# Kernel tuning notes

Measured on AMD Instinct MI355X. Metric: run time of the kernel, lower is better.

The kernel has to match this reference:

```python
import jax, jax.numpy as jnp
import numpy as np

# PEPS geometry (matches init_kwargs descriptor)
LX, LY, D, PHYS = 6, 6, 4, 2
BATCH = 1024


def _amplitude(T, xs):
    """Exact amplitude of one spin configuration.

    T : [Lx, Ly, d, D, D, D, D] site tensors, bond axes ordered (up, right, down, left).
    xs: [Lx, Ly] int spin configuration.
    Boundary (dangling) bonds of the open-boundary PEPS are index 0 of the
    corresponding axis (sliced away), exactly reproducing quimb's isel +
    contract_boundary_from_ymin/ymax (chi chosen >= exact rank) + contract.
    """
    ii = jnp.arange(LX)[:, None]
    jj = jnp.arange(LY)[None, :]
    A = T[ii, jj, xs]  # gather physical index -> [Lx, Ly, D, D, D, D]

    def site(i, j):
        a = A[i, j]  # [u, r, dn, l]
        if i == 0:
            a = a[0:1]            # top row: up bond is trivial
        if i == LX - 1:
            a = a[:, :, 0:1]      # bottom row: down bond is trivial
        return a

    # --- boundary MPS from ymin: absorb columns 0 .. Ly/2-1 ---
    # env tensor per row: [a, h, b] with a/b vertical MPS bonds, h the
    # horizontal bond facing the next (rightward) column.
    L = [site(i, 0)[:, :, :, 0] for i in range(LX)]  # l bond trivial -> [u, r, dn]
    for j in range(1, LY // 2):
        newL = []
        for i in range(LX):
            e = jnp.einsum('alb,urdl->aurbd', L[i], site(i, j))
            a, u, r, b, d = e.shape
            newL.append(e.reshape(a * u, r, b * d))
        L = newL

    # --- boundary MPS from ymax: absorb columns Ly-1 .. Ly/2 ---
    R = [jnp.transpose(site(i, LY - 1)[:, 0], (0, 2, 1)) for i in range(LX)]  # [u, l, dn]
    for j in range(LY - 2, LY // 2 - 1, -1):
        newR = []
        for i in range(LX):
            e = jnp.einsum('ahb,uhdl->aulbd', R[i], site(i, j))
            a, u, l, b, d = e.shape
            newR.append(e.reshape(a * u, l, b * d))
        R = newR

    # --- zip the two boundary MPS together row by row ---
    v = jnp.ones((1, 1), dtype=T.dtype)
    for i in range(LX):
        v = jnp.einsum('xy,xhz,yhw->zw', v, L[i], R[i])
    return v[0, 0]


def setup_inputs() -> dict:
    key = jax.random.key(0)
    k1, k2 = jax.random.split(key)
    # 0.35 scale keeps the product of 36 tensors numerically tame in fp32
    T = jax.random.normal(k1, (LX, LY, PHYS, D, D, D, D), dtype=jnp.float32) * 0.35
    x = jax.random.randint(k2, (BATCH, LX * LY), 0, PHYS, dtype=jnp.int32)
    return {"x": x, "T": T}


def reference(x, T):
    xs = x.reshape(-1, LX, LY)
    return jax.vmap(lambda s: _amplitude(T, s))(xs)  # [B] amplitudes
```

## Files before the change

### kernel.cpp

```cpp
#include <hip/hip_runtime.h>

#define NROW 6
#define NCOL 6
#define BATCH 1024
#define NSITE 36

__device__ __forceinline__ int SWZ(int a) { return a ^ (((a >> 5) & 7) << 2); }

typedef const float __attribute__((address_space(4))) * fcp;

__global__ void peps_reorder_kernel(const float* __restrict__ T,
                                    float* __restrict__ Tm)
{
    int idx = blockIdx.x * 256 + threadIdx.x;
    if (idx >= NSITE * 2 * 256) return;
    int i  = idx & 15;
    int o  = (idx >> 4) & 15;
    int sp = (idx >> 8) & 1;
    int st = idx >> 9;
    int g = i >> 2, x = i & 3, gp = o >> 2, z = o & 3;
    Tm[idx] = T[st * 512 + sp * 256 + x * 64 + gp * 16 + z * 4 + g];
}

template<int GIN, int GOUT, int XS, int ZS, bool C0>
__device__ __forceinline__ void do_step4(float* __restrict__ W, const fcp Msf,
                                         const int* __restrict__ A, int p4c,
                                         bool act)
{
    if (!act) return;
    float in_s[4][16];
    if (C0) {
        if (XS == 4) {
            #pragma unroll
            for (int i = 0; i < 4; ++i) {
                float4 q = *(const float4*)&W[A[i]];
                in_s[i][0] = q.x; in_s[i][1] = q.y;
                in_s[i][2] = q.z; in_s[i][3] = q.w;
            }
        } else {
            #pragma unroll
            for (int i = 0; i < 4; ++i) in_s[i][0] = W[A[i]];
        }
    } else if (ZS == 4) {
        #pragma unroll
        for (int g = 0; g < GIN; ++g)
            #pragma unroll
            for (int x = 0; x < XS; ++x) {
                float4 q = *(const float4*)&W[A[x] + g * 4096];
                in_s[0][g*4+x] = q.x; in_s[1][g*4+x] = q.y;
                in_s[2][g*4+x] = q.z; in_s[3][g*4+x] = q.w;
            }
    } else {
        #pragma unroll
        for (int g = 0; g < GIN; ++g)
            #pragma unroll
            for (int x = 0; x < XS; ++x)
                #pragma unroll
                for (int i = 0; i < 4; ++i)
                    in_s[i][g*4+x] = W[SWZ(x * p4c + A[i]) + g * 4096];
    }
    #pragma unroll
    for (int gp = 0; gp < GOUT; ++gp) {
        float a[ZS][4];
        #pragma unroll
        for (int z = 0; z < ZS; ++z) {
            const int mb = (gp * 4 + z) * 16;
            #pragma unroll
            for (int i = 0; i < 4; ++i) a[z][i] = 0.f;
            #pragma unroll
            for (int g = 0; g < GIN; ++g)
                #pragma unroll
                for (int x = 0; x < XS; ++x) {
                    const float m = Msf[mb + g * 4 + x];
                    #pragma unroll
                    for (int i = 0; i < 4; ++i)
                        a[z][i] += m * in_s[i][g*4+x];
                }
        }
        if (C0 && ZS == 4) {
            #pragma unroll
            for (int i = 0; i < 4; ++i)
                *(float4*)&W[A[i] + gp * 4096] =
                    make_float4(a[0][i], a[1][i], a[2][i], a[3][i]);
        } else if (ZS == 4) {
            #pragma unroll
            for (int z = 0; z < 4; ++z)
                *(float4*)&W[A[z] + gp * 4096] =
                    make_float4(a[z][0], a[z][1], a[z][2], a[z][3]);
        } else if (C0) {
            #pragma unroll
            for (int i = 0; i < 4; ++i) W[A[i] + gp * 4096] = a[0][i];
        } else {
            #pragma unroll
            for (int i = 0; i < 4; ++i) W[SWZ(A[i]) + gp * 4096] = a[0][i];
        }
    }
}

__global__ __launch_bounds__(256, 2)
void peps_amp_kernel(const int* __restrict__ X, const float* __restrict__ Tm,
                     float* __restrict__ out)
{
    __shared__ float W[16384];

    const int b = blockIdx.x;
    const int t = threadIdx.x;
    const int u0 = 4 * t;
    const int* xrow = X + b * NSITE;

    unsigned long long sm = 0ull;
    const int4* xp = (const int4*)xrow;
    #pragma unroll
    for (int k = 0; k < 9; ++k) {
        int4 v = xp[k];
        sm |= ((unsigned long long)(v.x & 1)) << (4 * k + 0);
        sm |= ((unsigned long long)(v.y & 1)) << (4 * k + 1);
        sm |= ((unsigned long long)(v.z & 1)) << (4 * k + 2);
        sm |= ((unsigned long long)(v.w & 1)) << (4 * k + 3);
    }
    {
        unsigned lo = __builtin_amdgcn_readfirstlane((int)(sm & 0xffffffffull));
        unsigned hi = __builtin_amdgcn_readfirstlane((int)(sm >> 32));
        sm = ((unsigned long long)hi << 32) | lo;
    }

    if (t == 0) W[0] = 1.0f;

    int step = 0;
    for (int row = 0; row < NROW; ++row) {
        const int xs = (row == 0) ? 1 : 4;
        const int zs = (row == NROW - 1) ? 1 : 4;
        for (int c = 0; c < NCOL; ++c, ++step) {
            const int lowb  = (zs == 4) ? 2 * c : 0;
            const int highb = (xs == 4) ? 2 * (5 - c) : 0;
            const int scount = 1 << (lowb + highb);
            const int p4c = 1 << (2 * c);
            const int lowmask = (1 << lowb) - 1;
            const bool act = (u0 < scount);

            const int spin = (int)((sm >> step) & 1ull);
            const fcp Msf = (fcp)(unsigned long long)
                (const void*)(Tm + (size_t)(step * 2 + spin) * 256);

            __syncthreads();

            int A[4];
            if (c == 0) {
                #pragma unroll
                for (int i = 0; i < 4; ++i) A[i] = SWZ(16 * t + 4 * i);
            } else if (zs == 4) {
                const int mr0 = ((u0 >> lowb) << (2 * c + 2)) | (u0 & lowmask);
                #pragma unroll
                for (int d = 0; d < 4; ++d) A[d] = SWZ(d * p4c + mr0);
            } else {
                #pragma unroll
                for (int i = 0; i < 4; ++i) A[i] = (u0 + i) << (2 * c + 2);
            }

            if (row == 0) {
                if (c == 0)            do_step4<1,4,1,4,true >(W, Msf, A, p4c, act);
                else if (c < NCOL - 1) do_step4<4,4,1,4,false>(W, Msf, A, p4c, act);
                else                   do_step4<4,1,1,4,false>(W, Msf, A, p4c, act);
            } else if (row < NROW - 1) {
                if (c == 0)            do_step4<1,4,4,4,true >(W, Msf, A, p4c, act);
                else if (c < NCOL - 1) do_step4<4,4,4,4,false>(W, Msf, A, p4c, act);
                else                   do_step4<4,1,4,4,false>(W, Msf, A, p4c, act);
            } else {
                if (c == 0)            do_step4<1,4,4,1,true >(W, Msf, A, p4c, act);
                else if (c < NCOL - 1) do_step4<4,4,4,1,false>(W, Msf, A, p4c, act);
                else                   do_step4<4,1,4,1,false>(W, Msf, A, p4c, act);
            }
        }
    }
    __syncthreads();
    if (t == 0) out[b] = W[0];
}

extern "C" void kernel_launch(void* const* d_in, const int* in_sizes, int n_in,
                              void* d_out, int out_size, void* d_ws, size_t ws_size,
                              hipStream_t stream) {
    const int*   X  = (const int*)d_in[0];
    const float* Tg = (const float*)d_in[1];
    float* out = (float*)d_out;
    float* Tm  = (float*)d_ws;
    (void)in_sizes; (void)n_in; (void)ws_size; (void)out_size;
    peps_reorder_kernel<<<dim3(72), dim3(256), 0, stream>>>(Tg, Tm);
    peps_amp_kernel<<<dim3(BATCH), dim3(256), 0, stream>>>(X, Tm, out);
}
```

Measured before the change: 200.7 us.

## Fuse pairs of site contractions per thread to halve barrier count

Replaces the generic per-site step loop with specialized routines that contract two adjacent sites per thread while the intermediate stays in registers. This halves the number of shared-memory round trips and __syncthreads barriers per row. The first and last rows get dedicated small-thread-count code paths. The swizzle function gains an extra XOR term to reduce LDS bank conflicts for the new access strides. The cost is higher register pressure from the 64-element intermediates and more specialized code to maintain.

```diff
diff --git a/kernel.cpp b/kernel.cpp
--- a/kernel.cpp
+++ b/kernel.cpp
@@ -5,9 +5,18 @@
 #define BATCH 1024
 #define NSITE 36
 
-__device__ __forceinline__ int SWZ(int a) { return a ^ (((a >> 5) & 7) << 2); }
+__device__ __forceinline__ int SWZ(int a) {
+    return a ^ (((a >> 5) & 7) << 2) ^ (((a >> 8) & 3) << 3);
+}
 
 typedef const float __attribute__((address_space(4))) * fcp;
+
+__device__ __forceinline__ fcp msel(const float* Tm, int step,
+                                    unsigned long long sm) {
+    int spin = (int)((sm >> step) & 1ull);
+    return (fcp)(unsigned long long)(const void*)
+        (Tm + (size_t)(step * 2 + spin) * 256);
+}
 
 __global__ void peps_reorder_kernel(const float* __restrict__ T,
                                     float* __restrict__ Tm)
@@ -22,79 +31,92 @@
     Tm[idx] = T[st * 512 + sp * 256 + x * 64 + gp * 16 + z * 4 + g];
 }
 
-template<int GIN, int GOUT, int XS, int ZS, bool C0>
-__device__ __forceinline__ void do_step4(float* __restrict__ W, const fcp Msf,
-                                         const int* __restrict__ A, int p4c,
-                                         bool act)
+__device__ __forceinline__ void mid_first(float* __restrict__ W, fcp M0,
+                                          fcp M1, int base)
 {
-    if (!act) return;
-    float in_s[4][16];
-    if (C0) {
-        if (XS == 4) {
-            #pragma unroll
-            for (int i = 0; i < 4; ++i) {
-                float4 q = *(const float4*)&W[A[i]];
-                in_s[i][0] = q.x; in_s[i][1] = q.y;
-                in_s[i][2] = q.z; in_s[i][3] = q.w;
-            }
-        } else {
-            #pragma unroll
-            for (int i = 0; i < 4; ++i) in_s[i][0] = W[A[i]];
-        }
-    } else if (ZS == 4) {
-        #pragma unroll
-        for (int g = 0; g < GIN; ++g)
-            #pragma unroll
-            for (int x = 0; x < XS; ++x) {
-                float4 q = *(const float4*)&W[A[x] + g * 4096];
-                in_s[0][g*4+x] = q.x; in_s[1][g*4+x] = q.y;
-                in_s[2][g*4+x] = q.z; in_s[3][g*4+x] = q.w;
-            }
-    } else {
-        #pragma unroll
-        for (int g = 0; g < GIN; ++g)
-            #pragma unroll
-            for (int x = 0; x < XS; ++x)
-                #pragma unroll
-                for (int i = 0; i < 4; ++i)
-                    in_s[i][g*4+x] = W[SWZ(x * p4c + A[i]) + g * 4096];
-    }
-    #pragma unroll
-    for (int gp = 0; gp < GOUT; ++gp) {
-        float a[ZS][4];
-        #pragma unroll
-        for (int z = 0; z < ZS; ++z) {
-            const int mb = (gp * 4 + z) * 16;
-            #pragma unroll
-            for (int i = 0; i < 4; ++i) a[z][i] = 0.f;
-            #pragma unroll
-            for (int g = 0; g < GIN; ++g)
-                #pragma unroll
-                for (int x = 0; x < XS; ++x) {
-                    const float m = Msf[mb + g * 4 + x];
-                    #pragma unroll
-                    for (int i = 0; i < 4; ++i)
-                        a[z][i] += m * in_s[i][g*4+x];
-                }
-        }
-        if (C0 && ZS == 4) {
-            #pragma unroll
-            for (int i = 0; i < 4; ++i)
-                *(float4*)&W[A[i] + gp * 4096] =
-                    make_float4(a[0][i], a[1][i], a[2][i], a[3][i]);
-        } else if (ZS == 4) {
-            #pragma unroll
-            for (int z = 0; z < 4; ++z)
-                *(float4*)&W[A[z] + gp * 4096] =
-                    make_float4(a[z][0], a[z][1], a[z][2], a[z][3]);
-        } else if (C0) {
-            #pragma unroll
-            for (int i = 0; i < 4; ++i) W[A[i] + gp * 4096] = a[0][i];
-        } else {
-            #pragma unroll
-            for (int i = 0; i < 4; ++i) W[SWZ(A[i]) + gp * 4096] = a[0][i];
-        }
-    }
+    float U[4][4];
+    #pragma unroll
+    for (int x1 = 0; x1 < 4; ++x1) {
+        float4 q = *(const float4*)&W[SWZ(base + 4 * x1)];
+        U[x1][0] = q.x; U[x1][1] = q.y; U[x1][2] = q.z; U[x1][3] = q.w;
+    }
+    float V[4][4][4];
+    #pragma unroll
+    for (int gp = 0; gp < 4; ++gp)
+        #pragma unroll
+        for (int z0 = 0; z0 < 4; ++z0)
+            #pragma unroll
+            for (int x1 = 0; x1 < 4; ++x1) {
+                float acc = 0.f;
+                #pragma unroll
+                for (int x0 = 0; x0 < 4; ++x0)
+                    acc += M0[(gp * 4 + z0) * 16 + x0] * U[x1][x0];
+                V[gp][z0][x1] = acc;
+            }
+    #pragma unroll
+    for (int gp1 = 0; gp1 < 4; ++gp1)
+        #pragma unroll
+        for (int z1 = 0; z1 < 4; ++z1) {
+            float o[4];
+            #pragma unroll
+            for (int z0 = 0; z0 < 4; ++z0) {
+                float acc = 0.f;
+                #pragma unroll
+                for (int gp = 0; gp < 4; ++gp)
+                    #pragma unroll
+                    for (int x1 = 0; x1 < 4; ++x1)
+                        acc += M1[(gp1 * 4 + z1) * 16 + gp * 4 + x1]
+                             * V[gp][z0][x1];
+                o[z0] = acc;
+            }
+            *(float4*)&W[gp1 * 4096 + SWZ(base + 4 * z1)] =
+                make_float4(o[0], o[1], o[2], o[3]);
+        }
+}
+
+template<int S, bool LAST>
+__device__ __forceinline__ void mid_pair(float* __restrict__ W, fcp Ma, fcp Mb,
+                                         int base)
+{
+    float U[4][4][4];
+    #pragma unroll
+    for (int g = 0; g < 4; ++g)
+        #pragma unroll
+        for (int xa = 0; xa < 4; ++xa)
+            #pragma unroll
+            for (int xb = 0; xb < 4; ++xb)
+                U[g][xa][xb] = W[g * 4096 + SWZ(base + S * xa + 4 * S * xb)];
+    float V[4][4][4];
+    #pragma unroll
+    for (int gp = 0; gp < 4; ++gp)
+        #pragma unroll
+        for (int za = 0; za < 4; ++za)
+            #pragma unroll
+            for (int xb = 0; xb < 4; ++xb) {
+                float acc = 0.f;
+                #pragma unroll
+                for (int g = 0; g < 4; ++g)
+                    #pragma unroll
+                    for (int xa = 0; xa < 4; ++xa)
+                        acc += Ma[(gp * 4 + za) * 16 + g * 4 + xa]
+                             * U[g][xa][xb];
+                V[gp][za][xb] = acc;
+            }
+    #pragma unroll
+    for (int gb = 0; gb < (LAST ? 1 : 4); ++gb)
+        #pragma unroll
+        for (int zb = 0; zb < 4; ++zb)
+            #pragma unroll
+            for (int za = 0; za < 4; ++za) {
+                float acc = 0.f;
+                #pragma unroll
+                for (int gp = 0; gp < 4; ++gp)
+                    #pragma unroll
+                    for (int xb = 0; xb < 4; ++xb)
+                        acc += Mb[(gb * 4 + zb) * 16 + gp * 4 + xb]
+                             * V[gp][za][xb];
+                W[gb * 4096 + SWZ(base + S * za + 4 * S * zb)] = acc;
+            }
 }
 
 __global__ __launch_bounds__(256, 2)
@@ -105,7 +127,6 @@
 
     const int b = blockIdx.x;
     const int t = threadIdx.x;
-    const int u0 = 4 * t;
     const int* xrow = X + b * NSITE;
 
     unsigned long long sm = 0ull;
@@ -124,56 +145,192 @@
         sm = ((unsigned long long)hi << 32) | lo;
     }
 
-    if (t == 0) W[0] = 1.0f;
-
-    int step = 0;
-    for (int row = 0; row < NROW; ++row) {
-        const int xs = (row == 0) ? 1 : 4;
-        const int zs = (row == NROW - 1) ? 1 : 4;
-        for (int c = 0; c < NCOL; ++c, ++step) {
-            const int lowb  = (zs == 4) ? 2 * c : 0;
-            const int highb = (xs == 4) ? 2 * (5 - c) : 0;
-            const int scount = 1 << (lowb + highb);
-            const int p4c = 1 << (2 * c);
-            const int lowmask = (1 << lowb) - 1;
-            const bool act = (u0 < scount);
-
-            const int spin = (int)((sm >> step) & 1ull);
-            const fcp Msf = (fcp)(unsigned long long)
-                (const void*)(Tm + (size_t)(step * 2 + spin) * 256);
-
-            __syncthreads();
-
-            int A[4];
-            if (c == 0) {
-                #pragma unroll
-                for (int i = 0; i < 4; ++i) A[i] = SWZ(16 * t + 4 * i);
-            } else if (zs == 4) {
-                const int mr0 = ((u0 >> lowb) << (2 * c + 2)) | (u0 & lowmask);
-                #pragma unroll
-                for (int d = 0; d < 4; ++d) A[d] = SWZ(d * p4c + mr0);
-            } else {
-                #pragma unroll
-                for (int i = 0; i < 4; ++i) A[i] = (u0 + i) << (2 * c + 2);
-            }
-
-            if (row == 0) {
-                if (c == 0)            do_step4<1,4,1,4,true >(W, Msf, A, p4c, act);
-                else if (c < NCOL - 1) do_step4<4,4,1,4,false>(W, Msf, A, p4c, act);
-                else                   do_step4<4,1,1,4,false>(W, Msf, A, p4c, act);
-            } else if (row < NROW - 1) {
-                if (c == 0)            do_step4<1,4,4,4,true >(W, Msf, A, p4c, act);
-                else if (c < NCOL - 1) do_step4<4,4,4,4,false>(W, Msf, A, p4c, act);
-                else                   do_step4<4,1,4,4,false>(W, Msf, A, p4c, act);
-            } else {
-                if (c == 0)            do_step4<1,4,4,1,true >(W, Msf, A, p4c, act);
-                else if (c < NCOL - 1) do_step4<4,4,4,1,false>(W, Msf, A, p4c, act);
-                else                   do_step4<4,1,4,1,false>(W, Msf, A, p4c, act);
-            }
-        }
-    }
-    __syncthreads();
-    if (t == 0) out[b] = W[0];
+    if (t == 0) {
+        fcp M0 = msel(Tm, 0, sm), M1 = msel(Tm, 1, sm);
+        float V[4][4];
+        #pragma unroll
+        for (int gp = 0; gp < 4; ++gp)
+            #pragma unroll
+            for (int z0 = 0; z0 < 4; ++z0)
+                V[gp][z0] = M0[(gp * 4 + z0) * 16];
+        #pragma unroll
+        for (int gp1 = 0; gp1 < 4; ++gp1)
+            #pragma unroll
+            for (int z1 = 0; z1 < 4; ++z1) {
+                float o[4];
+                #pragma unroll
+                for (int z0 = 0; z0 < 4; ++z0) {
+                    float acc = 0.f;
+                    #pragma unroll
+                    for (int gp = 0; gp < 4; ++gp)
+                        acc += M1[(gp1 * 4 + z1) * 16 + gp * 4] * V[gp][z0];
+                    o[z0] = acc;
+                }
+                *(float4*)&W[gp1 * 4096 + SWZ(4 * z1)] =
+                    make_float4(o[0], o[1], o[2], o[3]);
+            }
+    }
+    __syncthreads();
+    if (t < 16) {
+        fcp M2 = msel(Tm, 2, sm), M3 = msel(Tm, 3, sm);
+        float U[4];
+        #pragma unroll
+        for (int g = 0; g < 4; ++g) U[g] = W[g * 4096 + SWZ(t)];
+        float V[4][4];
+        #pragma unroll
+        for (int gp = 0; gp < 4; ++gp)
+            #pragma unroll
+            for (int z2 = 0; z2 < 4; ++z2) {
+                float acc = 0.f;
+                #pragma unroll
+                for (int g = 0; g < 4; ++g)
+                    acc += M2[(gp * 4 + z2) * 16 + g * 4] * U[g];
+                V[gp][z2] = acc;
+            }
+        #pragma unroll
+        for (int gp3 = 0; gp3 < 4; ++gp3)
+            #pragma unroll
+            for (int z3 = 0; z3 < 4; ++z3)
+                #pragma unroll
+                for (int z2 = 0; z2 < 4; ++z2) {
+                    float acc = 0.f;
+                    #pragma unroll
+                    for (int gp = 0; gp < 4; ++gp)
+                        acc += M3[(gp3 * 4 + z3) * 16 + gp * 4] * V[gp][z2];
+                    W[gp3 * 4096 + SWZ(t + 16 * z2 + 64 * z3)] = acc;
+                }
+    }
+    __syncthreads();
+    {
+        fcp M4 = msel(Tm, 4, sm), M5 = msel(Tm, 5, sm);
+        float U[4];
+        #pragma unroll
+        for (int g = 0; g < 4; ++g) U[g] = W[g * 4096 + SWZ(t)];
+        float V[4][4];
+        #pragma unroll
+        for (int gp = 0; gp < 4; ++gp)
+            #pragma unroll
+            for (int z4 = 0; z4 < 4; ++z4) {
+                float acc = 0.f;
+                #pragma unroll
+                for (int g = 0; g < 4; ++g)
+                    acc += M4[(gp * 4 + z4) * 16 + g * 4] * U[g];
+                V[gp][z4] = acc;
+            }
+        #pragma unroll
+        for (int z5 = 0; z5 < 4; ++z5)
+            #pragma unroll
+            for (int z4 = 0; z4 < 4; ++z4) {
+                float acc = 0.f;
+                #pragma unroll
+                for (int gp = 0; gp < 4; ++gp)
+                    acc += M5[z5 * 16 + gp * 4] * V[gp][z4];
+                W[SWZ(t + 256 * z4 + 1024 * z5)] = acc;
+            }
+    }
+
+    #pragma unroll 1
+    for (int row = 1; row <= 4; ++row) {
+        const int s0 = row * 6;
+        __syncthreads();
+        mid_first(W, msel(Tm, s0, sm), msel(Tm, s0 + 1, sm), t << 4);
+        __syncthreads();
+        mid_pair<16, false>(W, msel(Tm, s0 + 2, sm), msel(Tm, s0 + 3, sm),
+                            (t & 15) | ((t >> 4) << 8));
+        __syncthreads();
+        mid_pair<256, true>(W, msel(Tm, s0 + 4, sm), msel(Tm, s0 + 5, sm), t);
+    }
+
+    __syncthreads();
+    {
+        fcp M0 = msel(Tm, 30, sm), M1 = msel(Tm, 31, sm);
+        const int base = t << 4;
+        float V[4][4];
+        #pragma unroll
+        for (int x1 = 0; x1 < 4; ++x1) {
+            float4 q = *(const float4*)&W[SWZ(base + 4 * x1)];
+            float U[4] = {q.x, q.y, q.z, q.w};
+            #pragma unroll
+            for (int gp = 0; gp < 4; ++gp) {
+                float acc = 0.f;
+                #pragma unroll
+                for (int x0 = 0; x0 < 4; ++x0)
+                    acc += M0[gp * 64 + x0] * U[x0];
+                V[gp][x1] = acc;
+            }
+        }
+        #pragma unroll
+        for (int gp1 = 0; gp1 < 4; ++gp1) {
+            float acc = 0.f;
+            #pragma unroll
+            for (int gp = 0; gp < 4; ++gp)
+                #pragma unroll
+                for (int x1 = 0; x1 < 4; ++x1)
+                    acc += M1[gp1 * 64 + gp * 4 + x1] * V[gp][x1];
+            W[gp1 * 4096 + SWZ(base)] = acc;
+        }
+    }
+    __syncthreads();
+    if (t < 16) {
+        fcp M2 = msel(Tm, 32, sm), M3 = msel(Tm, 33, sm);
+        float V[4][4];
+        #pragma unroll
+        for (int x3 = 0; x3 < 4; ++x3) {
+            #pragma unroll
+            for (int gp = 0; gp < 4; ++gp) V[gp][x3] = 0.f;
+            #pragma unroll
+            for (int x2 = 0; x2 < 4; ++x2) {
+                float U[4];
+                #pragma unroll
+                for (int g = 0; g < 4; ++g)
+                    U[g] = W[g * 4096 + SWZ((x2 + 4 * x3 + 16 * t) << 4)];
+                #pragma unroll
+                for (int gp = 0; gp < 4; ++gp)
+                    #pragma unroll
+                    for (int g = 0; g < 4; ++g)
+                        V[gp][x3] += M2[gp * 64 + g * 4 + x2] * U[g];
+            }
+        }
+        #pragma unroll
+        for (int gp3 = 0; gp3 < 4; ++gp3) {
+            float acc = 0.f;
+            #pragma unroll
+            for (int gp = 0; gp < 4; ++gp)
+                #pragma unroll
+                for (int x3 = 0; x3 < 4; ++x3)
+                    acc += M3[gp3 * 64 + gp * 4 + x3] * V[gp][x3];
+            W[gp3 * 4096 + SWZ(t << 8)] = acc;
+        }
+    }
+    __syncthreads();
+    if (t == 0) {
+        fcp M4 = msel(Tm, 34, sm), M5 = msel(Tm, 35, sm);
+        float V[4][4];
+        #pragma unroll
+        for (int x5 = 0; x5 < 4; ++x5) {
+            #pragma unroll
+            for (int gp = 0; gp < 4; ++gp) V[gp][x5] = 0.f;
+            #pragma unroll
+            for (int x4 = 0; x4 < 4; ++x4) {
+                float U[4];
+                #pragma unroll
+                for (int g = 0; g < 4; ++g)
+                    U[g] = W[g * 4096 + SWZ((x4 + 4 * x5) << 8)];
+                #pragma unroll
+                for (int gp = 0; gp < 4; ++gp)
+                    #pragma unroll
+                    for (int g = 0; g < 4; ++g)
+                        V[gp][x5] += M4[gp * 64 + g * 4 + x4] * U[g];
+            }
+        }
+        float r = 0.f;
+        #pragma unroll
+        for (int gp = 0; gp < 4; ++gp)
+            #pragma unroll
+            for (int x5 = 0; x5 < 4; ++x5)
+                r += M5[gp * 4 + x5] * V[gp][x5];
+        out[b] = r;
+    }
 }
 
 extern "C" void kernel_launch(void* const* d_in, const int* in_sizes, int n_in,
```

New measurement: 230.2 us. 1.15x slower.

## Stage per-row site matrices in LDS with prefetch, drop reorder kernel

Applied to the files above, without the earlier changes.

Removes the separate reorder kernel launch. Each block now gathers its spin-selected site matrices from global memory, transposing on the fly, into a double-buffered shared-memory staging area one row ahead, overlapping the global loads with the current row's compute. The inner loop reads matrix coefficients from LDS as float4 instead of using scalar constant-address-space loads. This costs 12 KB of extra LDS per block, which may reduce occupancy alongside the 64 KB W buffer, and it moves the matrix reads from scalar loads to LDS vector loads.

```diff
diff --git a/kernel.cpp b/kernel.cpp
--- a/kernel.cpp
+++ b/kernel.cpp
@@ -7,23 +7,33 @@
 
 __device__ __forceinline__ int SWZ(int a) { return a ^ (((a >> 5) & 7) << 2); }
 
-typedef const float __attribute__((address_space(4))) * fcp;
-
-__global__ void peps_reorder_kernel(const float* __restrict__ T,
-                                    float* __restrict__ Tm)
-{
-    int idx = blockIdx.x * 256 + threadIdx.x;
-    if (idx >= NSITE * 2 * 256) return;
-    int i  = idx & 15;
-    int o  = (idx >> 4) & 15;
-    int sp = (idx >> 8) & 1;
-    int st = idx >> 9;
-    int g = i >> 2, x = i & 3, gp = o >> 2, z = o & 3;
-    Tm[idx] = T[st * 512 + sp * 256 + x * 64 + gp * 16 + z * 4 + g];
+
+__device__ __forceinline__ void stage_load(const float* __restrict__ T,
+                                           unsigned long long sm, int row,
+                                           int t, float* __restrict__ mst)
+{
+    #pragma unroll
+    for (int k = 0; k < 6; ++k) {
+        const int st = row * 6 + k;
+        const int spin = (int)((sm >> st) & 1ull);
+        const int w = t;
+        const int src = (st * 2 + spin) * 256 + (w & 3) * 64
+                      + ((w >> 6) & 3) * 16 + ((w >> 4) & 3) * 4
+                      + ((w >> 2) & 3);
+        mst[k] = T[src];
+    }
+}
+
+__device__ __forceinline__ void stage_write(float* __restrict__ Mrow,
+                                            int t, const float* __restrict__ mst)
+{
+    #pragma unroll
+    for (int k = 0; k < 6; ++k) Mrow[k * 256 + t] = mst[k];
 }
 
 template<int GIN, int GOUT, int XS, int ZS, bool C0>
-__device__ __forceinline__ void do_step4(float* __restrict__ W, const fcp Msf,
+__device__ __forceinline__ void do_step4(float* __restrict__ W,
+                                         const float* __restrict__ Ml,
                                          const int* __restrict__ A, int p4c,
                                          bool act)
 {
@@ -68,14 +78,22 @@
             #pragma unroll
             for (int i = 0; i < 4; ++i) a[z][i] = 0.f;
             #pragma unroll
-            for (int g = 0; g < GIN; ++g)
+            for (int g = 0; g < GIN; ++g) {
+                float mv[4];
+                if (XS == 4) {
+                    float4 mq = *(const float4*)&Ml[mb + g * 4];
+                    mv[0] = mq.x; mv[1] = mq.y; mv[2] = mq.z; mv[3] = mq.w;
+                } else {
+                    mv[0] = Ml[mb + g * 4];
+                }
                 #pragma unroll
                 for (int x = 0; x < XS; ++x) {
-                    const float m = Msf[mb + g * 4 + x];
+                    const float m = mv[x];
                     #pragma unroll
                     for (int i = 0; i < 4; ++i)
                         a[z][i] += m * in_s[i][g*4+x];
                 }
+            }
         }
         if (C0 && ZS == 4) {
             #pragma unroll
@@ -98,10 +116,11 @@
 }
 
 __global__ __launch_bounds__(256, 2)
-void peps_amp_kernel(const int* __restrict__ X, const float* __restrict__ Tm,
+void peps_amp_kernel(const int* __restrict__ X, const float* __restrict__ T,
                      float* __restrict__ out)
 {
     __shared__ float W[16384];
+    __shared__ float Mb[2][6][256];
 
     const int b = blockIdx.x;
     const int t = threadIdx.x;
@@ -124,12 +143,18 @@
         sm = ((unsigned long long)hi << 32) | lo;
     }
 
+    float mst[6];
+    stage_load(T, sm, 0, t, mst);
+    stage_write(&Mb[0][0][0], t, mst);
     if (t == 0) W[0] = 1.0f;
 
     int step = 0;
     for (int row = 0; row < NROW; ++row) {
         const int xs = (row == 0) ? 1 : 4;
         const int zs = (row == NROW - 1) ? 1 : 4;
+        const bool haveNext = (row + 1 < NROW);
+        if (haveNext) stage_load(T, sm, row + 1, t, mst);
+
         for (int c = 0; c < NCOL; ++c, ++step) {
             const int lowb  = (zs == 4) ? 2 * c : 0;
             const int highb = (xs == 4) ? 2 * (5 - c) : 0;
@@ -138,11 +163,12 @@
             const int lowmask = (1 << lowb) - 1;
             const bool act = (u0 < scount);
 
-            const int spin = (int)((sm >> step) & 1ull);
-            const fcp Msf = (fcp)(unsigned long long)
-                (const void*)(Tm + (size_t)(step * 2 + spin) * 256);
-
             __syncthreads();
+
+            if (c == NCOL - 1 && haveNext)
+                stage_write(&Mb[(row + 1) & 1][0][0], t, mst);
+
+            const float* Ml = &Mb[row & 1][c][0];
 
             int A[4];
             if (c == 0) {
@@ -158,17 +184,17 @@
             }
 
             if (row == 0) {
-                if (c == 0)            do_step4<1,4,1,4,true >(W, Msf, A, p4c, act);
-                else if (c < NCOL - 1) do_step4<4,4,1,4,false>(W, Msf, A, p4c, act);
-                else                   do_step4<4,1,1,4,false>(W, Msf, A, p4c, act);
+                if (c == 0)            do_step4<1,4,1,4,true >(W, Ml, A, p4c, act);
+                else if (c < NCOL - 1) do_step4<4,4,1,4,false>(W, Ml, A, p4c, act);
+                else                   do_step4<4,1,1,4,false>(W, Ml, A, p4c, act);
             } else if (row < NROW - 1) {
-                if (c == 0)            do_step4<1,4,4,4,true >(W, Msf, A, p4c, act);
-                else if (c < NCOL - 1) do_step4<4,4,4,4,false>(W, Msf, A, p4c, act);
-                else                   do_step4<4,1,4,4,false>(W, Msf, A, p4c, act);
+                if (c == 0)            do_step4<1,4,4,4,true >(W, Ml, A, p4c, act);
+                else if (c < NCOL - 1) do_step4<4,4,4,4,false>(W, Ml, A, p4c, act);
+                else                   do_step4<4,1,4,4,false>(W, Ml, A, p4c, act);
             } else {
-                if (c == 0)            do_step4<1,4,4,1,true >(W, Msf, A, p4c, act);
-                else if (c < NCOL - 1) do_step4<4,4,4,1,false>(W, Msf, A, p4c, act);
-                else                   do_step4<4,1,4,1,false>(W, Msf, A, p4c, act);
+                if (c == 0)            do_step4<1,4,4,1,true >(W, Ml, A, p4c, act);
+                else if (c < NCOL - 1) do_step4<4,4,4,1,false>(W, Ml, A, p4c, act);
+                else                   do_step4<4,1,4,1,false>(W, Ml, A, p4c, act);
             }
         }
     }
@@ -182,8 +208,6 @@
     const int*   X  = (const int*)d_in[0];
     const float* Tg = (const float*)d_in[1];
     float* out = (float*)d_out;
-    float* Tm  = (float*)d_ws;
-    (void)in_sizes; (void)n_in; (void)ws_size; (void)out_size;
-    peps_reorder_kernel<<<dim3(72), dim3(256), 0, stream>>>(Tg, Tm);
-    peps_amp_kernel<<<dim3(BATCH), dim3(256), 0, stream>>>(X, Tm, out);
-}
+    (void)in_sizes; (void)n_in; (void)ws_size; (void)out_size; (void)d_ws;
+    peps_amp_kernel<<<dim3(BATCH), dim3(256), 0, stream>>>(X, Tg, out);
+}
```

Measured after the change: 207.2 us. 3.3% more time.
